# Kernel optimization log

Hardware: AMD Instinct MI355X
Metric: run time of the kernel (lower is better)

Reference implementation:

```python
import jax, jax.numpy as jnp
import numpy as np

HEADS = 16
D_MODEL = 1024
D_K = D_MODEL // HEADS


def setup_inputs() -> dict:
    key = jax.random.key(0)
    ks = jax.random.split(key, 11)
    B, S, D = 4, 2048, D_MODEL
    q = jax.random.normal(ks[0], (B, S, D), dtype=jnp.float32)
    k = jax.random.normal(ks[1], (B, S, D), dtype=jnp.float32)
    v = jax.random.normal(ks[2], (B, S, D), dtype=jnp.float32)
    s = 1.0 / np.sqrt(D)
    Wq = jax.random.normal(ks[3], (D, D), dtype=jnp.float32) * s
    bq = jax.random.normal(ks[4], (D,), dtype=jnp.float32) * 0.01
    Wk = jax.random.normal(ks[5], (D, D), dtype=jnp.float32) * s
    bk = jax.random.normal(ks[6], (D,), dtype=jnp.float32) * 0.01
    Wv = jax.random.normal(ks[7], (D, D), dtype=jnp.float32) * s
    bv = jax.random.normal(ks[8], (D,), dtype=jnp.float32) * 0.01
    Wo = jax.random.normal(ks[9], (D, D), dtype=jnp.float32) * s
    bo = jax.random.normal(ks[10], (D,), dtype=jnp.float32) * 0.01
    return {"q": q, "k": k, "v": v, "Wq": Wq, "bq": bq, "Wk": Wk, "bk": bk,
            "Wv": Wv, "bv": bv, "Wo": Wo, "bo": bo}


def reference(q, k, v, Wq, bq, Wk, bk, Wv, bv, Wo, bo):
    B, Sq, D = q.shape
    Sk = k.shape[1]
    # Linear projections (torch Linear: x @ W.T + b)
    q_ = (q @ Wq.T + bq).reshape(B, Sq, HEADS, D_K).transpose(0, 2, 1, 3)  # [B,H,Sq,Dk]
    k_ = (k @ Wk.T + bk).reshape(B, Sk, HEADS, D_K).transpose(0, 2, 1, 3)  # [B,H,Sk,Dk]
    v_ = (v @ Wv.T + bv).reshape(B, Sk, HEADS, D_K).transpose(0, 2, 1, 3)  # [B,H,Sk,Dk]
    scores = jnp.einsum("bhqd,bhkd->bhqk", q_, k_) / jnp.sqrt(jnp.float32(D_K))
    attn = jax.nn.softmax(scores, axis=-1)
    ctx = jnp.einsum("bhqk,bhkd->bhqd", attn, v_)  # [B,H,Sq,Dk]
    concat = ctx.transpose(0, 2, 1, 3).reshape(B, Sq, D)
    # dropout p=0 -> identity (eval)
    return concat @ Wo.T + bo
```

## Files before the change

kernel.cpp:

```cpp
#include <hip/hip_runtime.h>
#include <hip/hip_bf16.h>
#include <stdint.h>

typedef unsigned short u16;
typedef __attribute__((ext_vector_type(8))) short bf16x8;
typedef __attribute__((ext_vector_type(4))) float f32x4;
typedef __attribute__((ext_vector_type(16))) float f32x16;
typedef __attribute__((ext_vector_type(4))) int i32x4;
typedef __attribute__((ext_vector_type(4))) unsigned short us4;

#define BATCH 4
#define HEADS 16
#define SEQ   2048
#define DMODEL 1024
#define DK    64

__device__ __forceinline__ u16 f2bf(float f) {
  __hip_bfloat16 h = __float2bfloat16(f);
  return *reinterpret_cast<u16*>(&h);
}

__device__ __forceinline__ int cvtpk(float a, float b) {
  int r;
  asm("v_cvt_pk_bf16_f32 %0, %1, %2" : "=v"(r) : "v"(a), "v"(b));
  return r;
}

__device__ __forceinline__ void plswap(int& a, int& b) {
  asm volatile("v_permlane32_swap_b32 %0, %1" : "+v"(a), "+v"(b));
}

__device__ __forceinline__ void gload_lds16(const u16* g, u16* l) {
  __builtin_amdgcn_global_load_lds((const __attribute__((address_space(1))) void*)g,
                                   (__attribute__((address_space(3))) void*)l, 16, 0, 0);
}

__device__ __forceinline__ void cvt8(const float* __restrict__ in, u16* __restrict__ out, long i) {
  float4 a = *(const float4*)(in + i);
  float4 b = *(const float4*)(in + i + 4);
  int w0 = cvtpk(a.x, a.y), w1 = cvtpk(a.z, a.w);
  int w2 = cvtpk(b.x, b.y), w3 = cvtpk(b.z, b.w);
  i32x4 pk; pk[0] = w0; pk[1] = w1; pk[2] = w2; pk[3] = w3;
  *(i32x4*)(out + i) = pk;
}

__global__ void cvt_qkv(const float* __restrict__ q, const float* __restrict__ k,
                        const float* __restrict__ v, u16* __restrict__ qo,
                        u16* __restrict__ ko, u16* __restrict__ vo) {
  long i = ((long)blockIdx.x * blockDim.x + threadIdx.x) * 8;
  const int sel = blockIdx.y;
  const float* in = (sel == 0) ? q : (sel == 1) ? k : v;
  u16* out = (sel == 0) ? qo : (sel == 1) ? ko : vo;
  cvt8(in, out, i);
}

__global__ void cvt_w(const float* __restrict__ w0, const float* __restrict__ w1,
                      const float* __restrict__ w2, const float* __restrict__ w3,
                      u16* __restrict__ o0, u16* __restrict__ o1,
                      u16* __restrict__ o2, u16* __restrict__ o3) {
  long i = ((long)blockIdx.x * blockDim.x + threadIdx.x) * 8;
  const int sel = blockIdx.y;
  const float* in = (sel == 0) ? w0 : (sel == 1) ? w1 : (sel == 2) ? w2 : w3;
  u16* out = (sel == 0) ? o0 : (sel == 1) ? o1 : (sel == 2) ? o2 : o3;
  cvt8(in, out, i);
}

template<int OUT_F32>
__global__ __launch_bounds__(256)
void gemm_bt(const u16* __restrict__ A, const u16* __restrict__ Bm,
             const float* __restrict__ bias, void* __restrict__ Cout,
             int M, int N, int K, float oscale) {
  __shared__ u16 As[128 * 64];
  __shared__ u16 Bs[128 * 64];
  const int tid = threadIdx.x;
  const int lane = tid & 63;
  const int w = tid >> 6;
  const int wr = w >> 1, wc = w & 1;
  const int lr = lane & 15, lg = lane >> 4;

  const int nwg = gridDim.x * gridDim.y;
  const int wg = blockIdx.y * gridDim.x + blockIdx.x;
  const int swz = (wg & 7) * (nwg >> 3) + (wg >> 3);
  const int bcol = swz % gridDim.x;
  const int brow = swz / gridDim.x;

  const size_t aBase = (size_t)(brow * 128) * K;
  const size_t bBase = (size_t)(bcol * 128) * K;

  int srow[4], scol[4];
#pragma unroll
  for (int j = 0; j < 4; j++) {
    const int c = tid + j * 256;
    srow[j] = c >> 3;
    scol[j] = ((c & 7) ^ (srow[j] & 7)) * 8;
  }

  f32x4 acc[4][4] = {};

  for (int k0 = 0; k0 < K; k0 += 64) {
#pragma unroll
    for (int j = 0; j < 4; j++) {
      const int c = tid + j * 256;
      gload_lds16(A + aBase + (size_t)srow[j] * K + k0 + scol[j], As + c * 8);
      gload_lds16(Bm + bBase + (size_t)srow[j] * K + k0 + scol[j], Bs + c * 8);
    }
    __syncthreads();
#pragma unroll
    for (int h = 0; h < 2; h++) {
      bf16x8 a[4], b[4];
#pragma unroll
      for (int i = 0; i < 4; i++) {
        const int row = wr * 64 + i * 16 + lr;
        a[i] = *(const bf16x8*)&As[row * 64 + (((h * 4 + lg) ^ (row & 7)) * 8)];
      }
#pragma unroll
      for (int j = 0; j < 4; j++) {
        const int row = wc * 64 + j * 16 + lr;
        b[j] = *(const bf16x8*)&Bs[row * 64 + (((h * 4 + lg) ^ (row & 7)) * 8)];
      }
#pragma unroll
      for (int i = 0; i < 4; i++)
#pragma unroll
        for (int j = 0; j < 4; j++)
          acc[i][j] = __builtin_amdgcn_mfma_f32_16x16x32_bf16(a[i], b[j], acc[i][j], 0, 0, 0);
    }
    __syncthreads();
  }

#pragma unroll
  for (int j = 0; j < 4; j++) {
    const int col = bcol * 128 + wc * 64 + j * 16 + lr;
    const float bv = bias[col];
#pragma unroll
    for (int i = 0; i < 4; i++) {
      const int row0 = brow * 128 + wr * 64 + i * 16 + lg * 4;
#pragma unroll
      for (int r = 0; r < 4; r++) {
        float v = (acc[i][j][r] + bv) * oscale;
        if (OUT_F32)
          ((float*)Cout)[(size_t)(row0 + r) * N + col] = v;
        else
          ((u16*)Cout)[(size_t)(row0 + r) * N + col] = f2bf(v);
      }
    }
  }
}

__global__ __launch_bounds__(256)
void transpose_v(const u16* __restrict__ Vp, u16* __restrict__ Vt) {
  __shared__ u16 t[64][68];
  const int bh = blockIdx.y, s0 = blockIdx.x * 64;
  const int b = bh >> 4, h = bh & 15;
  const int r = threadIdx.x >> 4, c4 = (threadIdx.x & 15) * 4;
#pragma unroll
  for (int rr = r; rr < 64; rr += 16)
    *(us4*)&t[rr][c4] = *(const us4*)&Vp[(size_t)(b * SEQ + s0 + rr) * DMODEL + h * DK + c4];
  __syncthreads();
#pragma unroll
  for (int dd = r; dd < 64; dd += 16) {
    us4 o;
    o[0] = t[c4 + 0][dd];
    o[1] = t[c4 + 1][dd];
    o[2] = t[c4 + 2][dd];
    o[3] = t[c4 + 3][dd];
    *(us4*)&Vt[(size_t)(bh * DK + dd) * SEQ + s0 + c4] = o;
  }
}

__device__ __forceinline__ void pack_group(const float* p, int* pw) {
  int W0 = cvtpk(p[0], p[1]);
  int W1 = cvtpk(p[2], p[3]);
  int W2 = cvtpk(p[4], p[5]);
  int W3 = cvtpk(p[6], p[7]);
  plswap(W0, W2);
  plswap(W1, W3);
  pw[0] = W0; pw[1] = W1; pw[2] = W2; pw[3] = W3;
}

__global__ __launch_bounds__(256, 4)
void attn2(const u16* __restrict__ Qp, const u16* __restrict__ Kp,
           const u16* __restrict__ Vt, u16* __restrict__ ctx) {
  __shared__ __align__(16) u16 smem[16384];
  const int tid = threadIdx.x;
  const int lane = tid & 63, w = tid >> 6;
  const int hi = lane >> 5;
  const int l31 = lane & 31;
  const int bh = blockIdx.y;
  const int b = bh >> 4, h = bh & 15;
  const int q0 = blockIdx.x * 128 + w * 32;

  const u16* qrow = Qp + (size_t)(b * SEQ + q0 + l31) * DMODEL + h * DK + hi * 8;
  bf16x8 qf[4];
#pragma unroll
  for (int kk = 0; kk < 4; kk++) qf[kk] = *(const bf16x8*)(qrow + kk * 16);

  const int srow = tid >> 3;
  const int scb = tid & 7;
  const int scol = (scb ^ (srow & 7)) * 8;
  const u16* kp = Kp + (size_t)(b * SEQ + srow) * DMODEL + h * DK + scol;
  const u16* vp = Vt + (size_t)bh * DK * SEQ + (size_t)srow * SEQ + scol;

  const int ksw = (l31 & 7) << 3;

  f32x16 o0 = {}, o1 = {};
  float lacc[4] = {};
  const int NT = SEQ / 64;

  {
    u16* Kd = smem;
    u16* Vd = smem + 4096;
    gload_lds16(kp, Kd + tid * 8);
    gload_lds16(kp + 32 * DMODEL, Kd + tid * 8 + 2048);
    gload_lds16(vp, Vd + tid * 8);
    gload_lds16(vp + 32 * SEQ, Vd + tid * 8 + 2048);
    kp += 64 * DMODEL;
    vp += 64;
  }
  __syncthreads();

  for (int t = 0; t < NT; ++t) {
    const int p = t & 1;
    if (t + 1 < NT) {
      u16* Kd = smem + ((p ^ 1) << 13);
      u16* Vd = Kd + 4096;
      gload_lds16(kp, Kd + tid * 8);
      gload_lds16(kp + 32 * DMODEL, Kd + tid * 8 + 2048);
      gload_lds16(vp, Vd + tid * 8);
      gload_lds16(vp + 32 * SEQ, Vd + tid * 8 + 2048);
      kp += 64 * DMODEL;
      vp += 64;
    }

    const u16* Kc = smem + (p << 13);
    const u16* Vc = Kc + 4096;

    f32x16 st0 = {}, st1 = {};
    __builtin_amdgcn_s_setprio(1);
#pragma unroll
    for (int kk = 0; kk < 4; kk++) {
      const int slot = (((kk * 2 + hi) << 3) ^ ksw);
      bf16x8 k0 = *(const bf16x8*)&Kc[l31 * 64 + slot];
      bf16x8 k1 = *(const bf16x8*)&Kc[(l31 + 32) * 64 + slot];
      st0 = __builtin_amdgcn_mfma_f32_32x32x16_bf16(k0, qf[kk], st0, 0, 0, 0);
      st1 = __builtin_amdgcn_mfma_f32_32x32x16_bf16(k1, qf[kk], st1, 0, 0, 0);
    }
    __builtin_amdgcn_s_setprio(0);

#pragma unroll
    for (int i = 0; i < 16; i++) st0[i] = __builtin_amdgcn_exp2f(st0[i]);
#pragma unroll
    for (int i = 0; i < 16; i++) st1[i] = __builtin_amdgcn_exp2f(st1[i]);
    float ts[8];
#pragma unroll
    for (int i = 0; i < 8; i++) ts[i] = (st0[i] + st0[i + 8]) + (st1[i] + st1[i + 8]);
#pragma unroll
    for (int i = 0; i < 4; i++) lacc[i] += ts[i] + ts[i + 4];

    int pw[4][4];
    {
      float tmp[8];
#pragma unroll
      for (int i = 0; i < 8; i++) tmp[i] = st0[i];
      pack_group(tmp, pw[0]);
#pragma unroll
      for (int i = 0; i < 8; i++) tmp[i] = st0[i + 8];
      pack_group(tmp, pw[1]);
#pragma unroll
      for (int i = 0; i < 8; i++) tmp[i] = st1[i];
      pack_group(tmp, pw[2]);
#pragma unroll
      for (int i = 0; i < 8; i++) tmp[i] = st1[i + 8];
      pack_group(tmp, pw[3]);
    }

    __builtin_amdgcn_s_setprio(1);
#pragma unroll
    for (int c = 0; c < 4; c++) {
      i32x4 pwv;
      pwv[0] = pw[c][0]; pwv[1] = pw[c][1]; pwv[2] = pw[c][2]; pwv[3] = pw[c][3];
      bf16x8 pf = __builtin_bit_cast(bf16x8, pwv);
      const int slot = (((c * 2 + hi) << 3) ^ ksw);
      bf16x8 v0 = *(const bf16x8*)&Vc[l31 * 64 + slot];
      bf16x8 v1 = *(const bf16x8*)&Vc[(l31 + 32) * 64 + slot];
      o0 = __builtin_amdgcn_mfma_f32_32x32x16_bf16(v0, pf, o0, 0, 0, 0);
      o1 = __builtin_amdgcn_mfma_f32_32x32x16_bf16(v1, pf, o1, 0, 0, 0);
    }
    __builtin_amdgcn_s_setprio(0);

    __syncthreads();
  }

  float lsum = (lacc[0] + lacc[1]) + (lacc[2] + lacc[3]);
  lsum += __shfl_xor(lsum, 32);
  const float rl = 1.0f / lsum;
  u16* ot = smem + w * (32 * 72);
#pragma unroll
  for (int ds_ = 0; ds_ < 2; ds_++) {
#pragma unroll
    for (int g = 0; g < 4; g++) {
#pragma unroll
      for (int pr = 0; pr < 2; pr++) {
        const int r = g * 4 + pr * 2;
        const int d = ds_ * 32 + (r & 3) + 8 * (r >> 2) + 4 * hi;
        float e0 = (ds_ ? o1[r] : o0[r]) * rl;
        float e1 = (ds_ ? o1[r + 1] : o0[r + 1]) * rl;
        *(int*)&ot[l31 * 72 + d] = cvtpk(e0, e1);
      }
    }
  }
  __syncthreads();
  const int rq = lane >> 3;
  const int rc = (lane & 7) * 8;
#pragma unroll
  for (int it = 0; it < 4; ++it) {
    const int qq = it * 8 + rq;
    bf16x8 vrow = *(const bf16x8*)&ot[qq * 72 + rc];
    *(bf16x8*)&ctx[(size_t)(b * SEQ + q0 + qq) * DMODEL + h * DK + rc] = vrow;
  }
}

extern "C" void kernel_launch(void* const* d_in, const int* in_sizes, int n_in,
                              void* d_out, int out_size, void* d_ws, size_t ws_size,
                              hipStream_t stream) {
  const float* q  = (const float*)d_in[0];
  const float* k  = (const float*)d_in[1];
  const float* v  = (const float*)d_in[2];
  const float* Wq = (const float*)d_in[3];
  const float* bq = (const float*)d_in[4];
  const float* Wk = (const float*)d_in[5];
  const float* bk = (const float*)d_in[6];
  const float* Wv = (const float*)d_in[7];
  const float* bv = (const float*)d_in[8];
  const float* Wo = (const float*)d_in[9];
  const float* bo = (const float*)d_in[10];

  char* ws = (char*)d_ws;
  const size_t MB = 1024 * 1024;
  u16* qb  = (u16*)(ws + 0 * MB);
  u16* kb  = (u16*)(ws + 16 * MB);
  u16* vb  = (u16*)(ws + 32 * MB);
  u16* Wqb = (u16*)(ws + 48 * MB);
  u16* Wkb = (u16*)(ws + 50 * MB);
  u16* Wvb = (u16*)(ws + 52 * MB);
  u16* Wob = (u16*)(ws + 54 * MB);
  u16* Qp  = (u16*)(ws + 56 * MB);
  u16* Kp  = (u16*)(ws + 72 * MB);
  u16* Vp  = (u16*)(ws + 88 * MB);
  u16* Vt  = (u16*)(ws + 104 * MB);
  u16* ctx = (u16*)(ws + 120 * MB);

  const long nIn = (long)BATCH * SEQ * DMODEL;
  const long nW  = (long)DMODEL * DMODEL;

  cvt_qkv<<<dim3(nIn / 8 / 256, 3), 256, 0, stream>>>(q, k, v, qb, kb, vb);
  cvt_w<<<dim3(nW / 8 / 256, 4), 256, 0, stream>>>(Wq, Wk, Wv, Wo, Wqb, Wkb, Wvb, Wob);

  dim3 gGemm(DMODEL / 128, BATCH * SEQ / 128);
  const float qscale = 0.125f * 1.44269504088896340736f;
  gemm_bt<0><<<gGemm, 256, 0, stream>>>(qb, Wqb, bq, Qp, BATCH * SEQ, DMODEL, DMODEL, qscale);
  gemm_bt<0><<<gGemm, 256, 0, stream>>>(kb, Wkb, bk, Kp, BATCH * SEQ, DMODEL, DMODEL, 1.f);
  gemm_bt<0><<<gGemm, 256, 0, stream>>>(vb, Wvb, bv, Vp, BATCH * SEQ, DMODEL, DMODEL, 1.f);

  transpose_v<<<dim3(SEQ / 64, BATCH * HEADS), 256, 0, stream>>>(Vp, Vt);
  attn2<<<dim3(SEQ / 128, BATCH * HEADS), 256, 0, stream>>>(Qp, Kp, Vt, ctx);

  gemm_bt<1><<<gGemm, 256, 0, stream>>>(ctx, Wob, bo, (float*)d_out, BATCH * SEQ, DMODEL, DMODEL, 1.f);
}
```

Before: 220.5 us.

## Fuse QKV projections into one GEMM launch with in-epilogue V transpose

Merges the three Q/K/V projection GEMMs into a single launch of 1536 workgroups that picks its operand set by column group. The V branch's epilogue writes the tile transposed through LDS straight into the Vt layout, which removes the separate transpose kernel and the Vp round trip. The two conversion kernels are also merged into one launch, in which the weight-sized slices exit early. This cuts launch count and intermediate memory traffic, at the cost of a branchy epilogue and idle blocks in the conversion kernel.

New measurement: 207.1 us. -6.1%, faster.

```diff
diff --git a/kernel.cpp b/kernel.cpp
--- a/kernel.cpp
+++ b/kernel.cpp
@@ -14,6 +14,7 @@
 #define SEQ   2048
 #define DMODEL 1024
 #define DK    64
+#define QSCALE (0.125f * 1.44269504088896340736f)
 
 __device__ __forceinline__ u16 f2bf(float f) {
   __hip_bfloat16 h = __float2bfloat16(f);
@@ -38,38 +39,152 @@
 __device__ __forceinline__ void cvt8(const float* __restrict__ in, u16* __restrict__ out, long i) {
   float4 a = *(const float4*)(in + i);
   float4 b = *(const float4*)(in + i + 4);
-  int w0 = cvtpk(a.x, a.y), w1 = cvtpk(a.z, a.w);
-  int w2 = cvtpk(b.x, b.y), w3 = cvtpk(b.z, b.w);
-  i32x4 pk; pk[0] = w0; pk[1] = w1; pk[2] = w2; pk[3] = w3;
+  i32x4 pk;
+  pk[0] = cvtpk(a.x, a.y); pk[1] = cvtpk(a.z, a.w);
+  pk[2] = cvtpk(b.x, b.y); pk[3] = cvtpk(b.z, b.w);
   *(i32x4*)(out + i) = pk;
 }
 
-__global__ void cvt_qkv(const float* __restrict__ q, const float* __restrict__ k,
-                        const float* __restrict__ v, u16* __restrict__ qo,
-                        u16* __restrict__ ko, u16* __restrict__ vo) {
+__global__ void cvt_all(const float* __restrict__ q, const float* __restrict__ k,
+                        const float* __restrict__ v, const float* __restrict__ w0,
+                        const float* __restrict__ w1, const float* __restrict__ w2,
+                        const float* __restrict__ w3, u16* __restrict__ qo,
+                        u16* __restrict__ ko, u16* __restrict__ vo,
+                        u16* __restrict__ o0, u16* __restrict__ o1,
+                        u16* __restrict__ o2, u16* __restrict__ o3) {
+  const int sel = blockIdx.y;
   long i = ((long)blockIdx.x * blockDim.x + threadIdx.x) * 8;
-  const int sel = blockIdx.y;
-  const float* in = (sel == 0) ? q : (sel == 1) ? k : v;
-  u16* out = (sel == 0) ? qo : (sel == 1) ? ko : vo;
+  if (sel >= 3 && i >= (long)DMODEL * DMODEL) return;
+  const float* in = (sel == 0) ? q : (sel == 1) ? k : (sel == 2) ? v
+                  : (sel == 3) ? w0 : (sel == 4) ? w1 : (sel == 5) ? w2 : w3;
+  u16* out = (sel == 0) ? qo : (sel == 1) ? ko : (sel == 2) ? vo
+           : (sel == 3) ? o0 : (sel == 4) ? o1 : (sel == 5) ? o2 : o3;
   cvt8(in, out, i);
 }
 
-__global__ void cvt_w(const float* __restrict__ w0, const float* __restrict__ w1,
-                      const float* __restrict__ w2, const float* __restrict__ w3,
-                      u16* __restrict__ o0, u16* __restrict__ o1,
-                      u16* __restrict__ o2, u16* __restrict__ o3) {
-  long i = ((long)blockIdx.x * blockDim.x + threadIdx.x) * 8;
-  const int sel = blockIdx.y;
-  const float* in = (sel == 0) ? w0 : (sel == 1) ? w1 : (sel == 2) ? w2 : w3;
-  u16* out = (sel == 0) ? o0 : (sel == 1) ? o1 : (sel == 2) ? o2 : o3;
-  cvt8(in, out, i);
-}
-
-template<int OUT_F32>
+__global__ __launch_bounds__(256)
+void gemm_qkv(const u16* __restrict__ qb, const u16* __restrict__ kb,
+              const u16* __restrict__ vb, const u16* __restrict__ Wqb,
+              const u16* __restrict__ Wkb, const u16* __restrict__ Wvb,
+              const float* __restrict__ bq, const float* __restrict__ bk,
+              const float* __restrict__ bv, u16* __restrict__ Qp,
+              u16* __restrict__ Kp, u16* __restrict__ Vt) {
+  __shared__ u16 smem[128 * 64 * 2];
+  u16* As = smem;
+  u16* Bs = smem + 128 * 64;
+  const int K = DMODEL;
+  const int tid = threadIdx.x;
+  const int lane = tid & 63;
+  const int w = tid >> 6;
+  const int wr = w >> 1, wc = w & 1;
+  const int lr = lane & 15, lg = lane >> 4;
+
+  const int wg = blockIdx.y * 24 + blockIdx.x;
+  const int swz = (wg & 7) * (1536 >> 3) + (wg >> 3);
+  const int bcolg = swz % 24;
+  const int brow = swz / 24;
+  const int sel = bcolg >> 3;
+  const int bcol = bcolg & 7;
+
+  const u16* A  = (sel == 0) ? qb : (sel == 1) ? kb : vb;
+  const u16* Bm = (sel == 0) ? Wqb : (sel == 1) ? Wkb : Wvb;
+  const float* bias = (sel == 0) ? bq : (sel == 1) ? bk : bv;
+
+  const size_t aBase = (size_t)(brow * 128) * K;
+  const size_t bBase = (size_t)(bcol * 128) * K;
+
+  int srow[4], scol[4];
+#pragma unroll
+  for (int j = 0; j < 4; j++) {
+    const int c = tid + j * 256;
+    srow[j] = c >> 3;
+    scol[j] = ((c & 7) ^ (srow[j] & 7)) * 8;
+  }
+
+  f32x4 acc[4][4] = {};
+
+  for (int k0 = 0; k0 < K; k0 += 64) {
+#pragma unroll
+    for (int j = 0; j < 4; j++) {
+      const int c = tid + j * 256;
+      gload_lds16(A + aBase + (size_t)srow[j] * K + k0 + scol[j], As + c * 8);
+      gload_lds16(Bm + bBase + (size_t)srow[j] * K + k0 + scol[j], Bs + c * 8);
+    }
+    __syncthreads();
+#pragma unroll
+    for (int h = 0; h < 2; h++) {
+      bf16x8 a[4], b[4];
+#pragma unroll
+      for (int i = 0; i < 4; i++) {
+        const int row = wr * 64 + i * 16 + lr;
+        a[i] = *(const bf16x8*)&As[row * 64 + (((h * 4 + lg) ^ (row & 7)) * 8)];
+      }
+#pragma unroll
+      for (int j = 0; j < 4; j++) {
+        const int row = wc * 64 + j * 16 + lr;
+        b[j] = *(const bf16x8*)&Bs[row * 64 + (((h * 4 + lg) ^ (row & 7)) * 8)];
+      }
+#pragma unroll
+      for (int i = 0; i < 4; i++)
+#pragma unroll
+        for (int j = 0; j < 4; j++)
+          acc[i][j] = __builtin_amdgcn_mfma_f32_16x16x32_bf16(a[i], b[j], acc[i][j], 0, 0, 0);
+    }
+    __syncthreads();
+  }
+
+  if (sel < 2) {
+    u16* Cout = (sel == 0) ? Qp : Kp;
+    const float oscale = (sel == 0) ? QSCALE : 1.f;
+#pragma unroll
+    for (int j = 0; j < 4; j++) {
+      const int col = bcol * 128 + wc * 64 + j * 16 + lr;
+      const float bv_ = bias[col];
+#pragma unroll
+      for (int i = 0; i < 4; i++) {
+        const int row0 = brow * 128 + wr * 64 + i * 16 + lg * 4;
+#pragma unroll
+        for (int r = 0; r < 4; r++)
+          Cout[(size_t)(row0 + r) * DMODEL + col] = f2bf((acc[i][j][r] + bv_) * oscale);
+      }
+    }
+  } else {
+    const int b = brow >> 4;
+    const int s0 = (brow & 15) * 128;
+#pragma unroll
+    for (int j = 0; j < 4; j++) {
+      const int col = wc * 64 + j * 16 + lr;
+      const int xsw = (col & 7) << 3;
+      const float bv_ = bias[bcol * 128 + col];
+#pragma unroll
+      for (int i = 0; i < 4; i++) {
+        const int row0 = wr * 64 + i * 16 + lg * 4;
+#pragma unroll
+        for (int pr = 0; pr < 2; pr++) {
+          float e0 = acc[i][j][pr * 2] + bv_;
+          float e1 = acc[i][j][pr * 2 + 1] + bv_;
+          *(int*)&smem[col * 128 + ((row0 + pr * 2) ^ xsw)] = cvtpk(e0, e1);
+        }
+      }
+    }
+    __syncthreads();
+    const int col = tid >> 1, h2 = tid & 1;
+    const int xsw = (col & 7) << 3;
+    const int c = bcol * 128 + col;
+    const int hh = c >> 6, dk = c & 63;
+    u16* dst = Vt + (size_t)((b * 16 + hh) * 64 + dk) * SEQ + s0 + h2 * 64;
+#pragma unroll
+    for (int jj = 0; jj < 8; jj++) {
+      bf16x8 vrow = *(const bf16x8*)&smem[col * 128 + ((h2 * 64 + jj * 8) ^ xsw)];
+      *(bf16x8*)(dst + jj * 8) = vrow;
+    }
+  }
+}
+
 __global__ __launch_bounds__(256)
 void gemm_bt(const u16* __restrict__ A, const u16* __restrict__ Bm,
-             const float* __restrict__ bias, void* __restrict__ Cout,
-             int M, int N, int K, float oscale) {
+             const float* __restrict__ bias, float* __restrict__ Cout,
+             int M, int N, int K) {
   __shared__ u16 As[128 * 64];
   __shared__ u16 Bs[128 * 64];
   const int tid = threadIdx.x;
@@ -135,35 +250,9 @@
     for (int i = 0; i < 4; i++) {
       const int row0 = brow * 128 + wr * 64 + i * 16 + lg * 4;
 #pragma unroll
-      for (int r = 0; r < 4; r++) {
-        float v = (acc[i][j][r] + bv) * oscale;
-        if (OUT_F32)
-          ((float*)Cout)[(size_t)(row0 + r) * N + col] = v;
-        else
-          ((u16*)Cout)[(size_t)(row0 + r) * N + col] = f2bf(v);
-      }
-    }
-  }
-}
-
-__global__ __launch_bounds__(256)
-void transpose_v(const u16* __restrict__ Vp, u16* __restrict__ Vt) {
-  __shared__ u16 t[64][68];
-  const int bh = blockIdx.y, s0 = blockIdx.x * 64;
-  const int b = bh >> 4, h = bh & 15;
-  const int r = threadIdx.x >> 4, c4 = (threadIdx.x & 15) * 4;
-#pragma unroll
-  for (int rr = r; rr < 64; rr += 16)
-    *(us4*)&t[rr][c4] = *(const us4*)&Vp[(size_t)(b * SEQ + s0 + rr) * DMODEL + h * DK + c4];
-  __syncthreads();
-#pragma unroll
-  for (int dd = r; dd < 64; dd += 16) {
-    us4 o;
-    o[0] = t[c4 + 0][dd];
-    o[1] = t[c4 + 1][dd];
-    o[2] = t[c4 + 2][dd];
-    o[3] = t[c4 + 3][dd];
-    *(us4*)&Vt[(size_t)(bh * DK + dd) * SEQ + s0 + c4] = o;
+      for (int r = 0; r < 4; r++)
+        Cout[(size_t)(row0 + r) * N + col] = acc[i][j][r] + bv;
+    }
   }
 }
 
@@ -345,24 +434,19 @@
   u16* Wob = (u16*)(ws + 54 * MB);
   u16* Qp  = (u16*)(ws + 56 * MB);
   u16* Kp  = (u16*)(ws + 72 * MB);
-  u16* Vp  = (u16*)(ws + 88 * MB);
   u16* Vt  = (u16*)(ws + 104 * MB);
   u16* ctx = (u16*)(ws + 120 * MB);
 
   const long nIn = (long)BATCH * SEQ * DMODEL;
-  const long nW  = (long)DMODEL * DMODEL;
-
-  cvt_qkv<<<dim3(nIn / 8 / 256, 3), 256, 0, stream>>>(q, k, v, qb, kb, vb);
-  cvt_w<<<dim3(nW / 8 / 256, 4), 256, 0, stream>>>(Wq, Wk, Wv, Wo, Wqb, Wkb, Wvb, Wob);
-
-  dim3 gGemm(DMODEL / 128, BATCH * SEQ / 128);
-  const float qscale = 0.125f * 1.44269504088896340736f;
-  gemm_bt<0><<<gGemm, 256, 0, stream>>>(qb, Wqb, bq, Qp, BATCH * SEQ, DMODEL, DMODEL, qscale);
-  gemm_bt<0><<<gGemm, 256, 0, stream>>>(kb, Wkb, bk, Kp, BATCH * SEQ, DMODEL, DMODEL, 1.f);
-  gemm_bt<0><<<gGemm, 256, 0, stream>>>(vb, Wvb, bv, Vp, BATCH * SEQ, DMODEL, DMODEL, 1.f);
-
-  transpose_v<<<dim3(SEQ / 64, BATCH * HEADS), 256, 0, stream>>>(Vp, Vt);
+
+  cvt_all<<<dim3(nIn / 8 / 256, 7), 256, 0, stream>>>(q, k, v, Wq, Wk, Wv, Wo,
+                                                      qb, kb, vb, Wqb, Wkb, Wvb, Wob);
+
+  gemm_qkv<<<dim3(24, 64), 256, 0, stream>>>(qb, kb, vb, Wqb, Wkb, Wvb,
+                                             bq, bk, bv, Qp, Kp, Vt);
+
   attn2<<<dim3(SEQ / 128, BATCH * HEADS), 256, 0, stream>>>(Qp, Kp, Vt, ctx);
 
-  gemm_bt<1><<<gGemm, 256, 0, stream>>>(ctx, Wob, bo, (float*)d_out, BATCH * SEQ, DMODEL, DMODEL, 1.f);
-}
+  gemm_bt<<<dim3(DMODEL / 128, BATCH * SEQ / 128), 256, 0, stream>>>(
+      ctx, Wob, bo, (float*)d_out, BATCH * SEQ, DMODEL, DMODEL);
+}
```
